# Performance work log

Measured on AMD Instinct MI355X. Metric: run time of the kernel, lower is better.

The kernel has to match this reference:

```python
import jax, jax.numpy as jnp
import numpy as np

N_USER = 150_000
M_ITEM = 30_000
N_NODES = N_USER + M_ITEM
D = 64                      # embedding_dim
N_LAYERS = 3                # gcn_layer_number
E = 600_000                 # user-item interactions (symmetric nnz = 2E)
B = 1024
NUM_RATE, NUM_GENRE, NUM_DIR, NUM_ACT = 6, 25, 2186, 8030
NUM_GENDER, NUM_AGE, NUM_OCC, NUM_ZIP = 2, 7, 21, 3402
H1, H2 = 64, 64             # first/second fc hidden dims
FC1_IN = D * 10


def setup_inputs() -> dict:
    key = jax.random.key(0)
    ks = jax.random.split(key, 24)
    # aux features: 0/1 values are valid indices for every categorical field
    aux_info = jax.random.randint(ks[0], (B, 10246), 0, 2, dtype=jnp.int32)
    user_ids = jax.random.randint(ks[1], (B,), 0, N_USER, dtype=jnp.int32)
    item_ids = jax.random.randint(ks[2], (B,), 0, M_ITEM, dtype=jnp.int32)
    # bipartite graph: random interactions, symmetric normalized adjacency
    u = jax.random.randint(ks[3], (E,), 0, N_USER, dtype=jnp.int32)
    i = jax.random.randint(ks[4], (E,), 0, M_ITEM, dtype=jnp.int32) + N_USER
    graph_row = jnp.concatenate([u, i])
    graph_col = jnpph = jnp.concatenate([i, u]) if False else jnp.concatenate([i, u])
    deg = jax.ops.segment_sum(jnp.ones((2 * E,), jnp.float32), graph_row, num_segments=N_NODES)
    dinv = jnp.where(deg > 0, jax.lax.rsqrt(jnp.maximum(deg, 1.0)), 0.0)
    graph_val = dinv[graph_row] * dinv[graph_col]
    s = 0.1
    nrm = lambda k, shp: (jax.random.normal(k, shp, jnp.float32) * s)
    return {
        "aux_info": aux_info, "user_ids": user_ids, "item_ids": item_ids,
        "graph_row": graph_row, "graph_col": graph_col, "graph_val": graph_val,
        "rate_tab": nrm(ks[5], (NUM_RATE, D)),
        "genre_W": nrm(ks[6], (NUM_GENRE, D)),
        "director_W": nrm(ks[7], (NUM_DIR, D)),
        "actor_W": nrm(ks[8], (NUM_ACT, D)),
        "gender_tab": nrm(ks[9], (NUM_GENDER, D)),
        "age_tab": nrm(ks[10], (NUM_AGE, D)),
        "occ_tab": nrm(ks[11], (NUM_OCC, D)),
        "area_tab": nrm(ks[12], (NUM_ZIP, D)),
        "user_rel": nrm(ks[13], (N_USER, D)),
        "item_rel": nrm(ks[14], (M_ITEM, D)),
        "fc1_W": nrm(ks[15], (FC1_IN, H1)), "fc1_b": jnp.zeros((H1,), jnp.float32),
        "fc2_W": nrm(ks[16], (H1, H2)), "fc2_b": jnp.zeros((H2,), jnp.float32),
        "out_W": nrm(ks[17], (H2, 1)), "out_b": jnp.zeros((1,), jnp.float32),
    }


def _lightgcn(user_rel, item_rel, row, col, val):
    # LightGCN: repeated SpMM D^-1/2 A D^-1/2 @ emb, mean over layer outputs
    emb = jnp.concatenate([user_rel, item_rel], axis=0)      # [N, D]
    acc = emb
    for _ in range(N_LAYERS):
        emb = jax.ops.segment_sum(val[:, None] * emb[col], row, num_segments=N_NODES)
        acc = acc + emb
    light = acc / (N_LAYERS + 1)
    return light[:N_USER], light[N_USER:]


def _multi_hot(idx_int, W):
    x = idx_int.astype(jnp.float32)
    return (x @ W) / jnp.sum(x, axis=1, keepdims=True)


def reference(aux_info, user_ids, item_ids, graph_row, graph_col, graph_val,
              rate_tab, genre_W, director_W, actor_W,
              gender_tab, age_tab, occ_tab, area_tab,
              user_rel, item_rel,
              fc1_W, fc1_b, fc2_W, fc2_b, out_W, out_b):
    rate_idx = aux_info[:, 0]
    genre_idx = aux_info[:, 1:26]
    director_idx = aux_info[:, 26:2212]
    actor_idx = aux_info[:, 2212:10242]
    gender_idx = aux_info[:, 10242]
    age_idx = aux_info[:, 10243]
    occ_idx = aux_info[:, 10244]
    area_idx = aux_info[:, 10245]

    item_emb = jnp.concatenate([
        rate_tab[rate_idx],
        _multi_hot(genre_idx, genre_W),
        _multi_hot(director_idx, director_W),
        _multi_hot(actor_idx, actor_W),
    ], axis=1)                                               # [B, 4D]
    user_emb = jnp.concatenate([
        gender_tab[gender_idx], age_tab[age_idx],
        occ_tab[occ_idx], area_tab[area_idx],
    ], axis=1)                                               # [B, 4D]

    all_users, all_items = _lightgcn(user_rel, item_rel, graph_row, graph_col, graph_val)
    X = jnp.concatenate([item_emb, user_emb,
                         all_users[user_ids], all_items[item_ids]], axis=1)  # [B, 10D]
    X = jax.nn.relu(X @ fc1_W + fc1_b)
    X = jax.nn.relu(X @ fc2_W + fc2_b)
    return X @ out_W + out_b                                 # [B, 1]
```

## Files before the change

### kernel.cpp

```cpp
#include <hip/hip_runtime.h>
#include <hip/hip_bf16.h>
#include <hip/hip_fp16.h>

#define N_USER 150000
#define M_ITEM 30000
#define N_NODES 180000
#define E2 1200000
#define BATCH 1024
#define AUX_W 10246
#define KP_G 32
#define KP_D 2208
#define KP_A 8064
#define NBKT 265
#define WT_BLKS 2576
#define BCNT_BLKS 293
#define MH_BLKS 672
#define CVT_BLKS 5625

typedef __attribute__((ext_vector_type(8))) short short8;
typedef __attribute__((ext_vector_type(8))) unsigned short ushort8_t;
typedef __attribute__((ext_vector_type(4))) float f32x4;

__device__ __forceinline__ int bucket_of(int r) {
    return r < N_USER ? (r >> 10) : 147 + ((r - N_USER) >> 8);
}

__device__ __forceinline__ int detect_f32(const void* probe) {
    float v = __bfloat162float(((const __hip_bfloat16*)probe)[threadIdx.x & 63]);
    unsigned long long m = __ballot(!(fabsf(v) < 1000.0f));
    return __popcll(m) > 8;
}

struct CvtSeg { const void* src; float* dst; int n; int blk0; };
struct CvtBatch { CvtSeg seg[16]; };

__global__ void __launch_bounds__(256) k_prep(CvtBatch cb, int cvtBlks,
                                              const void* Wg, const void* Wd, const void* Wa,
                                              unsigned short* WtG, unsigned short* WtD, unsigned short* WtA,
                                              const int* __restrict__ grow, int* __restrict__ bucket_tot,
                                              int* __restrict__ deg, const void* probe) {
    int blk = blockIdx.x, tid = threadIdx.x;
    if (blk < cvtBlks) {
        int isf32 = detect_f32(probe);
        int si = 0;
        #pragma unroll
        for (int i = 0; i < 16; ++i) if (blk >= cb.seg[i].blk0) si = i;
        const CvtSeg sg = cb.seg[si];
        int i = (blk - sg.blk0) * 256 + tid;
        if (i >= sg.n) return;
        if (isf32) sg.dst[i] = ((const float*)sg.src)[i];
        else       sg.dst[i] = __bfloat162float(((const __hip_bfloat16*)sg.src)[i]);
        return;
    }
    if (blk < cvtBlks + WT_BLKS) {
        int isf32 = detect_f32(probe);
        int t = (blk - cvtBlks) * 256 + tid;
        if (t >= (KP_G + KP_D + KP_A) * 64) return;
        int kp = t >> 6, n = t & 63;
        int k, K; const void* src; unsigned short* dst;
        if (kp < KP_G)              { k = kp;               K = 25;   src = Wg; dst = WtG; }
        else if (kp < KP_G + KP_D)  { k = kp - KP_G;        K = 2186; src = Wd; dst = WtD; }
        else                        { k = kp - KP_G - KP_D; K = 8030; src = Wa; dst = WtA; }
        unsigned short v = 0;
        if (k < K) {
            if (isf32) {
                __hip_bfloat16 h = __float2bfloat16(((const float*)src)[(size_t)k * 64 + n]);
                v = *(unsigned short*)&h;
            } else {
                v = ((const unsigned short*)src)[(size_t)k * 64 + n];
            }
        }
        dst[(((size_t)(k >> 5) * 64 + n) * 4 + ((k >> 3) & 3)) * 8 + (k & 7)] = v;
        return;
    }
    __shared__ int h[NBKT];
    for (int i = tid; i < NBKT; i += 256) h[i] = 0;
    __syncthreads();
    int idx0 = (blk - cvtBlks - WT_BLKS) * 4096;
    #pragma unroll
    for (int k = 0; k < 16; ++k) {
        int i = idx0 + k * 256 + tid;
        if (i < E2) {
            int r = grow[i];
            atomicAdd(&h[bucket_of(r)], 1);
            atomicAdd(&deg[r], 1);
        }
    }
    __syncthreads();
    for (int i = tid; i < NBKT; i += 256) if (h[i]) atomicAdd(&bucket_tot[i], h[i]);
}

__global__ void __launch_bounds__(512) k_bscan(const int* __restrict__ bucket_tot,
                                               int* __restrict__ bucket_base,
                                               int* __restrict__ bucketcur,
                                               const int* __restrict__ deg,
                                               float* __restrict__ dinv, float* __restrict__ dsq,
                                               float* __restrict__ gsc) {
    int tid = threadIdx.x;
    if (blockIdx.x > 0) {
        int r = (blockIdx.x - 1) * 512 + tid;
        float d = (float)deg[r];
        bool nz = d > 0.f;
        dinv[r] = nz ? rsqrtf(d) : 0.f;
        dsq[r]  = nz ? 1.f / d  : 0.f;
        gsc[r]  = nz ? sqrtf(d) : 0.f;
        return;
    }
    __shared__ int s[512];
    s[tid] = (tid < NBKT) ? bucket_tot[tid] : 0;
    __syncthreads();
    for (int off = 1; off < 512; off <<= 1) {
        int v = (tid >= off) ? s[tid - off] : 0;
        __syncthreads();
        s[tid] += v;
        __syncthreads();
    }
    int excl = tid ? s[tid - 1] : 0;
    bucket_base[tid] = excl;
    if (tid < NBKT) bucketcur[tid] = excl;
}

__device__ void mhgemm_body(int blk, const int* __restrict__ aux,
                            const unsigned short* __restrict__ WtG,
                            const unsigned short* __restrict__ WtD,
                            const unsigned short* __restrict__ WtA,
                            float* __restrict__ Xmh, float* __restrict__ cntf) {
    int seg, rb, k0, klen, Kseg, auxoff;
    const unsigned short* Wt;
    if (blk < 16)       { seg = 0; rb = blk;                      k0 = 0;              klen = 25;                  Kseg = 25;   auxoff = 1;    Wt = WtG; }
    else if (blk < 160) { int t = blk - 16;  seg = 1; rb = t & 15; k0 = (t >> 4) * 256; klen = min(256, 2186 - k0); Kseg = 2186; auxoff = 26;   Wt = WtD; }
    else                { int t = blk - 160; seg = 2; rb = t & 15; k0 = (t >> 4) * 256; klen = min(256, 8030 - k0); Kseg = 8030; auxoff = 2212; Wt = WtA; }
    int lane = threadIdx.x & 63, wave = threadIdx.x >> 6;
    int m = lane & 15, quad = lane >> 4;
    int row = rb * 64 + wave * 16 + m;
    const int* arow = aux + (size_t)row * AUX_W + auxoff;

    f32x4 acc0 = {0.f,0.f,0.f,0.f}, acc1 = acc0, acc2 = acc0, acc3 = acc0;
    int isum = 0;
    int nchunk = (klen + 31) >> 5;
    int pa[8], na[8];
    auto lda = [&](int kci, int (&A)[8]) {
        int kb = k0 + kci * 32 + quad * 8;
        if (kb + 8 <= Kseg) {
            #pragma unroll
            for (int j = 0; j < 8; ++j) A[j] = arow[kb + j];
        } else {
            #pragma unroll
            for (int j = 0; j < 8; ++j) A[j] = (kb + j < Kseg) ? arow[kb + j] : 0;
        }
    };
    lda(0, pa);
    for (int kci = 0; kci < nchunk; ++kci) {
        if (kci + 1 < nchunk) lda(kci + 1, na);
        union { unsigned u[4]; short8 s; } af;
        af.u[0] = (unsigned)pa[0] * 16256u + (unsigned)pa[1] * 0x3F800000u;
        af.u[1] = (unsigned)pa[2] * 16256u + (unsigned)pa[3] * 0x3F800000u;
        af.u[2] = (unsigned)pa[4] * 16256u + (unsigned)pa[5] * 0x3F800000u;
        af.u[3] = (unsigned)pa[6] * 16256u + (unsigned)pa[7] * 0x3F800000u;
        isum += pa[0] + pa[1] + pa[2] + pa[3] + pa[4] + pa[5] + pa[6] + pa[7];
        size_t kcg = (size_t)(k0 >> 5) + kci;
        const unsigned short* bp = Wt + ((kcg * 64 + m) * 4 + quad) * 8;
        short8 b0 = *(const short8*)(bp);
        short8 b1 = *(const short8*)(bp + 512);
        short8 b2 = *(const short8*)(bp + 1024);
        short8 b3 = *(const short8*)(bp + 1536);
        acc0 = __builtin_amdgcn_mfma_f32_16x16x32_bf16(af.s, b0, acc0, 0, 0, 0);
        acc1 = __builtin_amdgcn_mfma_f32_16x16x32_bf16(af.s, b1, acc1, 0, 0, 0);
        acc2 = __builtin_amdgcn_mfma_f32_16x16x32_bf16(af.s, b2, acc2, 0, 0, 0);
        acc3 = __builtin_amdgcn_mfma_f32_16x16x32_bf16(af.s, b3, acc3, 0, 0, 0);
        #pragma unroll
        for (int j = 0; j < 8; ++j) pa[j] = na[j];
    }
    float asum = (float)isum;
    asum += __shfl_xor(asum, 16);
    asum += __shfl_xor(asum, 32);
    if (quad == 0) atomicAdd(&cntf[seg * BATCH + row], asum);
    float* xbase = Xmh + ((size_t)seg * BATCH + rb * 64 + wave * 16 + quad * 4) * 64;
    #pragma unroll
    for (int reg = 0; reg < 4; ++reg) {
        float* xr = xbase + (size_t)reg * 64;
        atomicAdd(&xr[ 0 + m], acc0[reg]);
        atomicAdd(&xr[16 + m], acc1[reg]);
        atomicAdd(&xr[32 + m], acc2[reg]);
        atomicAdd(&xr[48 + m], acc3[reg]);
    }
}

__global__ void __launch_bounds__(256) k_p1(const int* __restrict__ grow, const int* __restrict__ gcol,
                                            int* __restrict__ bucketcur, int2* __restrict__ binned,
                                            const int* __restrict__ aux,
                                            const unsigned short* __restrict__ WtG,
                                            const unsigned short* __restrict__ WtD,
                                            const unsigned short* __restrict__ WtA,
                                            float* __restrict__ Xmh, float* __restrict__ cntf,
                                            const void* rawU, const void* rawI,
                                            const float* __restrict__ dinv,
                                            __half* __restrict__ emb) {
    int blk = blockIdx.x;
    if (blk < MH_BLKS) {
        mhgemm_body(blk, aux, WtG, WtD, WtA, Xmh, cntf);
        return;
    }
    if (blk < MH_BLKS + BCNT_BLKS) {
        __shared__ int h1[NBKT], base1[NBKT];
        int tid = threadIdx.x;
        for (int i = tid; i < NBKT; i += 256) h1[i] = 0;
        __syncthreads();
        int idx0 = (blk - MH_BLKS) * 4096;
        int r[16], c[16];
        #pragma unroll
        for (int k = 0; k < 16; ++k) {
            int i = idx0 + k * 256 + tid;
            if (i < E2) {
                r[k] = grow[i]; c[k] = gcol[i];
                atomicAdd(&h1[bucket_of(r[k])], 1);
            } else r[k] = -1;
        }
        __syncthreads();
        for (int i = tid; i < NBKT; i += 256) {
            base1[i] = h1[i] ? atomicAdd(&bucketcur[i], h1[i]) : 0;
            h1[i] = 0;
        }
        __syncthreads();
        #pragma unroll
        for (int k = 0; k < 16; ++k) {
            if (r[k] >= 0) {
                int b = bucket_of(r[k]);
                int p = base1[b] + atomicAdd(&h1[b], 1);
                binned[p] = make_int2(r[k], c[k]);
            }
        }
        return;
    }
    int isf32 = detect_f32(rawU);
    int q = (blk - MH_BLKS - BCNT_BLKS) * 256 + threadIdx.x;
    if (q >= N_NODES * 8) return;
    int r = q >> 3;
    const void* src; size_t qq;
    if (r < N_USER) { src = rawU; qq = (size_t)q; }
    else            { src = rawI; qq = (size_t)q - (size_t)N_USER * 8; }
    float d = dinv[r];
    float f[8];
    if (isf32) {
        float4 a = ((const float4*)src)[qq * 2], b = ((const float4*)src)[qq * 2 + 1];
        f[0]=a.x; f[1]=a.y; f[2]=a.z; f[3]=a.w; f[4]=b.x; f[5]=b.y; f[6]=b.z; f[7]=b.w;
    } else {
        ushort8_t u = ((const ushort8_t*)src)[qq];
        #pragma unroll
        for (int i = 0; i < 8; ++i) {
            unsigned short us = u[i];
            f[i] = __bfloat162float(*(__hip_bfloat16*)&us);
        }
    }
    ushort8_t o;
    #pragma unroll
    for (int i = 0; i < 8; ++i) {
        __half h = __float2half(f[i] * d);
        o[i] = *(unsigned short*)&h;
    }
    ((ushort8_t*)emb)[(size_t)q] = o;
}

__global__ void __launch_bounds__(256) k_p2(const int2* __restrict__ binned, const int* __restrict__ bb,
                                            int* __restrict__ cols, int2* __restrict__ moffs) {
    __shared__ int h[1024];
    __shared__ int ws2[256];
    int b = blockIdx.x, tid = threadIdx.x;
    int r0, r1;
    if (b < 147) { r0 = b << 10; r1 = min((b + 1) << 10, N_USER); }
    else         { r0 = N_USER + ((b - 147) << 8); r1 = min(N_USER + ((b - 146) << 8), N_NODES); }
    int s0 = bb[b], e0 = bb[b + 1];
    for (int i = tid; i < 1024; i += 256) h[i] = 0;
    __syncthreads();
    for (int j = s0 + tid; j < e0; j += 256) atomicAdd(&h[binned[j].x - r0], 1);
    __syncthreads();
    int t0 = tid * 4;
    int a0 = h[t0], a1 = h[t0 + 1], a2 = h[t0 + 2], a3 = h[t0 + 3];
    ws2[tid] = a0 + a1 + a2 + a3;
    __syncthreads();
    for (int off = 1; off < 256; off <<= 1) {
        int v = (tid >= off) ? ws2[tid - off] : 0;
        __syncthreads();
        ws2[tid] += v;
        __syncthreads();
    }
    int excl = tid ? ws2[tid - 1] : 0;
    int ex[4] = { excl, excl + a0, excl + a0 + a1, excl + a0 + a1 + a2 };
    int ac[4] = { a0, a1, a2, a3 };
    #pragma unroll
    for (int i = 0; i < 4; ++i) {
        int row = r0 + t0 + i;
        if (row < r1) moffs[row] = make_int2(s0 + ex[i], s0 + ex[i] + ac[i]);
        h[t0 + i] = ex[i];
    }
    __syncthreads();
    for (int j = s0 + tid; j < e0; j += 256) {
        int2 e = binned[j];
        int p = s0 + atomicAdd(&h[e.x - r0], 1);
        cols[p] = e.y << 7;
    }
}

__global__ void __launch_bounds__(256, 8) k_spmv(const __half* __restrict__ src, __half* __restrict__ dst,
                                                 const int2* __restrict__ moffs_in, const int* __restrict__ cols,
                                                 const float* __restrict__ dsq,
                                                 int spmvN, float* __restrict__ tacc,
                                                 const int* __restrict__ uids, const int* __restrict__ iids,
                                                 const float* __restrict__ gsc,
                                                 const void* rawU, const void* rawI,
                                                 int2* __restrict__ moffs2, int xmode) {
    int tid = threadIdx.x, lane = tid & 63;
    int blk = blockIdx.x;
    if (blk >= spmvN) {
        if (xmode == 1) {
            int t = (blk - spmvN) * 4 + (tid >> 6);
            int r = (t < BATCH) ? uids[t] : (N_USER + iids[t - BATCH]);
            tacc[(size_t)t * 64 + lane] += __half2float(src[(size_t)r * 64 + lane]) * gsc[r];
            return;
        }
        if (blk < spmvN + 512) {
            int t = (blk - spmvN) * 4 + (tid >> 6);
            int r = (t < BATCH) ? uids[t] : (N_USER + iids[t - BATCH]);
            int2 se = moffs_in[r];
            if (lane == 0) moffs2[r] = se;
            for (int j = se.x + lane; j < se.y; j += 64) {
                int c = (unsigned)cols[j] >> 7;
                moffs2[c] = moffs_in[c];
            }
            return;
        }
        {
            int isf32 = detect_f32(rawU);
            int t = (blk - spmvN - 512) * 4 + (tid >> 6);
            const void* s; size_t ri;
            if (t < BATCH) { s = rawU; ri = (size_t)uids[t]; }
            else           { s = rawI; ri = (size_t)iids[t - BATCH]; }
            float v;
            if (isf32) v = ((const float*)s)[ri * 64 + lane];
            else       v = __bfloat162float(((const __hip_bfloat16*)s)[ri * 64 + lane]);
            tacc[(size_t)t * 64 + lane] = v;
            return;
        }
    }
    int wid8 = blk * 4 + (tid >> 6);
    int g = lane >> 3, l8 = lane & 7;
    int r = wid8 * 8 + g;
    int2 se = moffs_in[r];
    int s = se.x, e = se.y;
    const char* sb = (const char*)src + (l8 << 4);
    float2 a0 = {0.f,0.f}, a1 = a0, a2 = a0, a3 = a0;
    int j0 = s;
    for (; j0 + 4 <= e; j0 += 4) {
        int c[4];
        #pragma unroll
        for (int u = 0; u < 4; ++u) c[u] = cols[j0 + u];
        float4 rv[4];
        #pragma unroll
        for (int u = 0; u < 4; ++u) rv[u] = *(const float4*)(sb + (size_t)(unsigned)c[u]);
        #pragma unroll
        for (int u = 0; u < 4; ++u) {
            const __half2* h = (const __half2*)&rv[u];
            float2 f0 = __half22float2(h[0]), f1 = __half22float2(h[1]);
            float2 f2 = __half22float2(h[2]), f3 = __half22float2(h[3]);
            a0.x += f0.x; a0.y += f0.y; a1.x += f1.x; a1.y += f1.y;
            a2.x += f2.x; a2.y += f2.y; a3.x += f3.x; a3.y += f3.y;
        }
    }
    if (j0 < e) {
        int c[4]; float w[4];
        #pragma unroll
        for (int u = 0; u < 4; ++u) {
            int j = j0 + u;
            c[u] = cols[min(j, e - 1)];
            w[u] = (j < e) ? 1.f : 0.f;
        }
        float4 rv[4];
        #pragma unroll
        for (int u = 0; u < 4; ++u) rv[u] = *(const float4*)(sb + (size_t)(unsigned)c[u]);
        #pragma unroll
        for (int u = 0; u < 4; ++u) {
            const __half2* h = (const __half2*)&rv[u];
            float2 f0 = __half22float2(h[0]), f1 = __half22float2(h[1]);
            float2 f2 = __half22float2(h[2]), f3 = __half22float2(h[3]);
            a0.x = fmaf(w[u], f0.x, a0.x); a0.y = fmaf(w[u], f0.y, a0.y);
            a1.x = fmaf(w[u], f1.x, a1.x); a1.y = fmaf(w[u], f1.y, a1.y);
            a2.x = fmaf(w[u], f2.x, a2.x); a2.y = fmaf(w[u], f2.y, a2.y);
            a3.x = fmaf(w[u], f3.x, a3.x); a3.y = fmaf(w[u], f3.y, a3.y);
        }
    }
    if (e > s) {
        float d = dsq[r];
        float4 ov;
        __half2* op = (__half2*)&ov;
        op[0] = __floats2half2_rn(a0.x * d, a0.y * d);
        op[1] = __floats2half2_rn(a1.x * d, a1.y * d);
        op[2] = __floats2half2_rn(a2.x * d, a2.y * d);
        op[3] = __floats2half2_rn(a3.x * d, a3.y * d);
        *(float4*)((char*)dst + ((size_t)r << 7) + (l8 << 4)) = ov;
    }
}

__global__ void __launch_bounds__(256) k_spmv3(const __half* __restrict__ src, float* __restrict__ tacc,
                                               const int2* __restrict__ moffs, const int* __restrict__ cols,
                                               const float* __restrict__ dinv, const float* __restrict__ gsc,
                                               const int* __restrict__ uids, const int* __restrict__ iids) {
    int tid = threadIdx.x, lane = tid & 63;
    int t = blockIdx.x * 4 + (tid >> 6);
    if (t >= 2048) return;
    int r = (t < BATCH) ? uids[t] : (N_USER + iids[t - BATCH]);
    int2 se = moffs[r];
    int s = se.x, e = se.y;
    int p = lane & 31, ep = lane >> 5;
    const char* sb = (const char*)src + (p << 2);
    float ax = 0.f, ay = 0.f;
    int j0 = s;
    for (; j0 + 16 <= e; j0 += 16) {
        int c[8];
        #pragma unroll
        for (int u = 0; u < 8; ++u) c[u] = cols[j0 + 2 * u + ep];
        float2 v[8];
        #pragma unroll
        for (int u = 0; u < 8; ++u) v[u] = __half22float2(*(const __half2*)(sb + (size_t)(unsigned)c[u]));
        #pragma unroll
        for (int u = 0; u < 8; ++u) { ax += v[u].x; ay += v[u].y; }
    }
    if (j0 + 8 <= e) {
        int c[4];
        #pragma unroll
        for (int u = 0; u < 4; ++u) c[u] = cols[j0 + 2 * u + ep];
        float2 v[4];
        #pragma unroll
        for (int u = 0; u < 4; ++u) v[u] = __half22float2(*(const __half2*)(sb + (size_t)(unsigned)c[u]));
        #pragma unroll
        for (int u = 0; u < 4; ++u) { ax += v[u].x; ay += v[u].y; }
        j0 += 8;
    }
    if (j0 + 4 <= e) {
        int c0 = cols[j0 + ep], c1 = cols[j0 + 2 + ep];
        float2 v0 = __half22float2(*(const __half2*)(sb + (size_t)(unsigned)c0));
        float2 v1 = __half22float2(*(const __half2*)(sb + (size_t)(unsigned)c1));
        ax += v0.x + v1.x; ay += v0.y + v1.y;
        j0 += 4;
    }
    if (j0 < e) {
        int j1 = j0 + ep, j2 = j0 + 2 + ep;
        int c0 = cols[min(j1, e - 1)], c1 = cols[min(j2, e - 1)];
        float w0 = (j1 < e) ? 1.f : 0.f, w1 = (j2 < e) ? 1.f : 0.f;
        float2 v0 = __half22float2(*(const __half2*)(sb + (size_t)(unsigned)c0));
        float2 v1 = __half22float2(*(const __half2*)(sb + (size_t)(unsigned)c1));
        ax = fmaf(w0, v0.x, ax); ay = fmaf(w0, v0.y, ay);
        ax = fmaf(w1, v1.x, ax); ay = fmaf(w1, v1.y, ay);
    }
    ax += __shfl_xor(ax, 32);
    ay += __shfl_xor(ay, 32);
    if (ep == 0) {
        float2 self = __half22float2(*(const __half2*)((const char*)src + ((size_t)r << 7) + (p << 2)));
        float di = dinv[r], g = gsc[r];
        float* tp = tacc + (size_t)t * 64 + (p << 1);
        tp[0] += di * ax + g * self.x;
        tp[1] += di * ay + g * self.y;
    }
}

__global__ void __launch_bounds__(256) k_mlp(const int* __restrict__ aux,
                                             const float* __restrict__ ratef, const float* __restrict__ genderf,
                                             const float* __restrict__ agef, const float* __restrict__ occf,
                                             const float* __restrict__ areaf, const float* __restrict__ tacc,
                                             const float* __restrict__ Xmh, const float* __restrict__ cntf,
                                             const float* __restrict__ W1, const float* __restrict__ b1,
                                             const float* __restrict__ W2, const float* __restrict__ b2,
                                             const float* __restrict__ Wo, const float* __restrict__ bo,
                                             void* __restrict__ out, const void* probe) {
    __shared__ float sx[4][640];
    __shared__ float sh[4][64];
    int isf32 = detect_f32(probe);
    int lane = threadIdx.x & 63, w = threadIdx.x >> 6;
    int b = blockIdx.x * 4 + w;
    const int* arow = aux + (size_t)b * AUX_W;
    float* xr = sx[w];
    xr[0   + lane] = ratef[arow[0] * 64 + lane];
    xr[64  + lane] = Xmh[((size_t)0 * BATCH + b) * 64 + lane] / cntf[0 * BATCH + b];
    xr[128 + lane] = Xmh[((size_t)1 * BATCH + b) * 64 + lane] / cntf[1 * BATCH + b];
    xr[192 + lane] = Xmh[((size_t)2 * BATCH + b) * 64 + lane] / cntf[2 * BATCH + b];
    xr[256 + lane] = genderf[arow[10242] * 64 + lane];
    xr[320 + lane] = agef[arow[10243] * 64 + lane];
    xr[384 + lane] = occf[arow[10244] * 64 + lane];
    xr[448 + lane] = areaf[arow[10245] * 64 + lane];
    xr[512 + lane] = tacc[(size_t)b * 64 + lane] * 0.25f;
    xr[576 + lane] = tacc[(size_t)(BATCH + b) * 64 + lane] * 0.25f;
    float acc = b1[lane];
    #pragma unroll 8
    for (int k = 0; k < 640; ++k) acc += xr[k] * W1[(size_t)k * 64 + lane];
    float h1 = fmaxf(acc, 0.f);
    sh[w][lane] = h1;
    float acc2 = b2[lane];
    #pragma unroll 8
    for (int j = 0; j < 64; ++j) acc2 += sh[w][j] * W2[(size_t)j * 64 + lane];
    float h2 = fmaxf(acc2, 0.f);
    float p = h2 * Wo[lane];
    #pragma unroll
    for (int off = 32; off; off >>= 1) p += __shfl_down(p, off);
    if (lane == 0) {
        float r = p + bo[0];
        if (isf32) ((float*)out)[b] = r;
        else       ((__hip_bfloat16*)out)[b] = __float2bfloat16(r);
    }
}

extern "C" void kernel_launch(void* const* d_in, const int* in_sizes, int n_in,
                              void* d_out, int out_size, void* d_ws, size_t ws_size,
                              hipStream_t stream) {
    const int* aux  = (const int*)d_in[0];
    const int* uids = (const int*)d_in[1];
    const int* iids = (const int*)d_in[2];
    const int* grow = (const int*)d_in[3];
    const int* gcol = (const int*)d_in[4];

    char* p = (char*)d_ws;
    auto alloc = [&](size_t bytes) -> char* {
        char* r = p;
        p += (bytes + 255) / 256 * 256;
        return r;
    };
    int*   bucket_tot  = (int*)alloc(512 * 4);
    float* Xmh         = (float*)alloc((size_t)3 * BATCH * 64 * 4);
    float* cntf        = (float*)alloc((size_t)3 * BATCH * 4);
    int2*  moffs2      = (int2*)alloc((size_t)180224 * 8);
    int*   deg         = (int*)alloc((size_t)180224 * 4);
    char*  zero_end    = p;
    int*   bucket_base = (int*)alloc(512 * 4);
    int*   bucketcur   = (int*)alloc(512 * 4);
    int2*  moffs       = (int2*)alloc((size_t)180224 * 8);
    float* dinv        = (float*)alloc((size_t)180224 * 4);
    float* dsq         = (float*)alloc((size_t)180224 * 4);
    float* gsc         = (float*)alloc((size_t)180224 * 4);
    int2*  binned      = (int2*)alloc((size_t)E2 * 8);
    int*   cols        = (int*)alloc((size_t)E2 * 4);
    __half* embA       = (__half*)alloc((size_t)N_NODES * 64 * 2);
    __half* embB       = (__half*)alloc((size_t)N_NODES * 64 * 2);
    float* tacc        = (float*)alloc((size_t)2048 * 64 * 4);
    unsigned short* WtG = (unsigned short*)alloc((size_t)KP_G * 64 * 2);
    unsigned short* WtD = (unsigned short*)alloc((size_t)KP_D * 64 * 2);
    unsigned short* WtA = (unsigned short*)alloc((size_t)KP_A * 64 * 2);
    float* ratef   = (float*)alloc(384 * 4);
    float* genderf = (float*)alloc(128 * 4);
    float* agef    = (float*)alloc(448 * 4);
    float* occf    = (float*)alloc(1344 * 4);
    float* areaf   = (float*)alloc((size_t)217728 * 4);
    float* fc1W    = (float*)alloc((size_t)40960 * 4);
    float* fc1b    = (float*)alloc(64 * 4);
    float* fc2W    = (float*)alloc(4096 * 4);
    float* fc2b    = (float*)alloc(64 * 4);
    float* outW    = (float*)alloc(64 * 4);
    float* outb    = (float*)alloc(4);

    const void* probe = d_in[14];

    hipMemsetAsync(bucket_tot, 0, (size_t)(zero_end - (char*)bucket_tot), stream);

    CvtBatch cb;
    int blk = 0, si = 0;
    auto addseg = [&](const void* s, float* d, int n) {
        cb.seg[si].src = s; cb.seg[si].dst = d; cb.seg[si].n = n; cb.seg[si].blk0 = blk;
        blk += (n + 255) / 256; ++si;
    };
    addseg(d_in[6],  ratef,   384);
    addseg(d_in[10], genderf, 128);
    addseg(d_in[11], agef,    448);
    addseg(d_in[12], occf,    1344);
    addseg(d_in[13], areaf,   217728);
    addseg(d_in[16], fc1W,   40960);
    addseg(d_in[17], fc1b,   64);
    addseg(d_in[18], fc2W,   4096);
    addseg(d_in[19], fc2b,   64);
    addseg(d_in[20], outW,   64);
    addseg(d_in[21], outb,   1);
    for (int i = si; i < 16; ++i) { cb.seg[i].src = nullptr; cb.seg[i].dst = nullptr; cb.seg[i].n = 0; cb.seg[i].blk0 = 0x7fffffff; }
    const int cvtBlks = blk;
    hipLaunchKernelGGL(k_prep, dim3(cvtBlks + WT_BLKS + BCNT_BLKS), dim3(256), 0, stream,
                       cb, cvtBlks, d_in[7], d_in[8], d_in[9], WtG, WtD, WtA, grow, bucket_tot, deg, probe);

    hipLaunchKernelGGL(k_bscan, dim3(353), dim3(512), 0, stream,
                       bucket_tot, bucket_base, bucketcur, deg, dinv, dsq, gsc);

    hipLaunchKernelGGL(k_p1, dim3(MH_BLKS + BCNT_BLKS + CVT_BLKS), dim3(256), 0, stream,
                       grow, gcol, bucketcur, binned, aux, WtG, WtD, WtA, Xmh, cntf,
                       d_in[14], d_in[15], dinv, embA);

    hipLaunchKernelGGL(k_p2, dim3(NBKT), dim3(256), 0, stream, binned, bucket_base, cols, moffs);

    const int spmvN = N_NODES / 32;
    hipLaunchKernelGGL(k_spmv, dim3(spmvN + 1024), dim3(256), 0, stream,
                       embA, embB, moffs, cols, dsq, spmvN, tacc, uids, iids, gsc,
                       d_in[14], d_in[15], moffs2, 0);
    hipLaunchKernelGGL(k_spmv, dim3(spmvN + 512), dim3(256), 0, stream,
                       embB, embA, moffs2, cols, dsq, spmvN, tacc, uids, iids, gsc,
                       d_in[14], d_in[15], moffs2, 1);
    hipLaunchKernelGGL(k_spmv3, dim3(2048 / 4), dim3(256), 0, stream,
                       embA, tacc, moffs, cols, dinv, gsc, uids, iids);

    hipLaunchKernelGGL(k_mlp, dim3(BATCH / 4), dim3(256), 0, stream,
                       aux, ratef, genderf, agef, occf, areaf, tacc, Xmh, cntf,
                       fc1W, fc1b, fc2W, fc2b, outW, outb, d_out, probe);
}
```

Measured before the change: 327.2 us.

## Derive node degrees from CSR build instead of global atomics

Drops the per-edge global atomicAdd on the degree array in the prep kernel and instead computes dinv, dsq and gsc inside the bucket-local CSR build kernel, where per-row counts are already known. The bucket-count blocks move to the front of the prep grid, the scan kernel shrinks to one block, and the embedding conversion is split out of k_p1 into its own kernel launched after k_p2. This removes 1.2M contended global atomics and a degree pass, at the cost of one extra kernel launch and serializing the embedding conversion behind the CSR build.

Result: faster. 290.4 us (-11.2%).

```diff
diff --git a/kernel.cpp b/kernel.cpp
--- a/kernel.cpp
+++ b/kernel.cpp
@@ -38,23 +38,38 @@
                                               const void* Wg, const void* Wd, const void* Wa,
                                               unsigned short* WtG, unsigned short* WtD, unsigned short* WtA,
                                               const int* __restrict__ grow, int* __restrict__ bucket_tot,
-                                              int* __restrict__ deg, const void* probe) {
+                                              const void* probe) {
     int blk = blockIdx.x, tid = threadIdx.x;
-    if (blk < cvtBlks) {
+    if (blk < BCNT_BLKS) {
+        __shared__ int h[NBKT];
+        for (int i = tid; i < NBKT; i += 256) h[i] = 0;
+        __syncthreads();
+        int idx0 = blk * 4096;
+        #pragma unroll
+        for (int k = 0; k < 16; ++k) {
+            int i = idx0 + k * 256 + tid;
+            if (i < E2) atomicAdd(&h[bucket_of(grow[i])], 1);
+        }
+        __syncthreads();
+        for (int i = tid; i < NBKT; i += 256) if (h[i]) atomicAdd(&bucket_tot[i], h[i]);
+        return;
+    }
+    if (blk < BCNT_BLKS + cvtBlks) {
         int isf32 = detect_f32(probe);
+        int cblk = blk - BCNT_BLKS;
         int si = 0;
         #pragma unroll
-        for (int i = 0; i < 16; ++i) if (blk >= cb.seg[i].blk0) si = i;
+        for (int i = 0; i < 16; ++i) if (cblk >= cb.seg[i].blk0) si = i;
         const CvtSeg sg = cb.seg[si];
-        int i = (blk - sg.blk0) * 256 + tid;
+        int i = (cblk - sg.blk0) * 256 + tid;
         if (i >= sg.n) return;
         if (isf32) sg.dst[i] = ((const float*)sg.src)[i];
         else       sg.dst[i] = __bfloat162float(((const __hip_bfloat16*)sg.src)[i]);
         return;
     }
-    if (blk < cvtBlks + WT_BLKS) {
+    {
         int isf32 = detect_f32(probe);
-        int t = (blk - cvtBlks) * 256 + tid;
+        int t = (blk - BCNT_BLKS - cvtBlks) * 256 + tid;
         if (t >= (KP_G + KP_D + KP_A) * 64) return;
         int kp = t >> 6, n = t & 63;
         int k, K; const void* src; unsigned short* dst;
@@ -71,42 +86,14 @@
             }
         }
         dst[(((size_t)(k >> 5) * 64 + n) * 4 + ((k >> 3) & 3)) * 8 + (k & 7)] = v;
-        return;
-    }
-    __shared__ int h[NBKT];
-    for (int i = tid; i < NBKT; i += 256) h[i] = 0;
-    __syncthreads();
-    int idx0 = (blk - cvtBlks - WT_BLKS) * 4096;
-    #pragma unroll
-    for (int k = 0; k < 16; ++k) {
-        int i = idx0 + k * 256 + tid;
-        if (i < E2) {
-            int r = grow[i];
-            atomicAdd(&h[bucket_of(r)], 1);
-            atomicAdd(&deg[r], 1);
-        }
-    }
-    __syncthreads();
-    for (int i = tid; i < NBKT; i += 256) if (h[i]) atomicAdd(&bucket_tot[i], h[i]);
+    }
 }
 
 __global__ void __launch_bounds__(512) k_bscan(const int* __restrict__ bucket_tot,
                                                int* __restrict__ bucket_base,
-                                               int* __restrict__ bucketcur,
-                                               const int* __restrict__ deg,
-                                               float* __restrict__ dinv, float* __restrict__ dsq,
-                                               float* __restrict__ gsc) {
+                                               int* __restrict__ bucketcur) {
+    __shared__ int s[512];
     int tid = threadIdx.x;
-    if (blockIdx.x > 0) {
-        int r = (blockIdx.x - 1) * 512 + tid;
-        float d = (float)deg[r];
-        bool nz = d > 0.f;
-        dinv[r] = nz ? rsqrtf(d) : 0.f;
-        dsq[r]  = nz ? 1.f / d  : 0.f;
-        gsc[r]  = nz ? sqrtf(d) : 0.f;
-        return;
-    }
-    __shared__ int s[512];
     s[tid] = (tid < NBKT) ? bucket_tot[tid] : 0;
     __syncthreads();
     for (int off = 1; off < 512; off <<= 1) {
@@ -192,48 +179,96 @@
                                             const unsigned short* __restrict__ WtG,
                                             const unsigned short* __restrict__ WtD,
                                             const unsigned short* __restrict__ WtA,
-                                            float* __restrict__ Xmh, float* __restrict__ cntf,
-                                            const void* rawU, const void* rawI,
-                                            const float* __restrict__ dinv,
-                                            __half* __restrict__ emb) {
+                                            float* __restrict__ Xmh, float* __restrict__ cntf) {
     int blk = blockIdx.x;
     if (blk < MH_BLKS) {
         mhgemm_body(blk, aux, WtG, WtD, WtA, Xmh, cntf);
         return;
     }
-    if (blk < MH_BLKS + BCNT_BLKS) {
-        __shared__ int h1[NBKT], base1[NBKT];
-        int tid = threadIdx.x;
-        for (int i = tid; i < NBKT; i += 256) h1[i] = 0;
+    __shared__ int h1[NBKT], base1[NBKT];
+    int tid = threadIdx.x;
+    for (int i = tid; i < NBKT; i += 256) h1[i] = 0;
+    __syncthreads();
+    int idx0 = (blk - MH_BLKS) * 4096;
+    int r[16], c[16];
+    #pragma unroll
+    for (int k = 0; k < 16; ++k) {
+        int i = idx0 + k * 256 + tid;
+        if (i < E2) {
+            r[k] = grow[i]; c[k] = gcol[i];
+            atomicAdd(&h1[bucket_of(r[k])], 1);
+        } else r[k] = -1;
+    }
+    __syncthreads();
+    for (int i = tid; i < NBKT; i += 256) {
+        base1[i] = h1[i] ? atomicAdd(&bucketcur[i], h1[i]) : 0;
+        h1[i] = 0;
+    }
+    __syncthreads();
+    #pragma unroll
+    for (int k = 0; k < 16; ++k) {
+        if (r[k] >= 0) {
+            int b = bucket_of(r[k]);
+            int p = base1[b] + atomicAdd(&h1[b], 1);
+            binned[p] = make_int2(r[k], c[k]);
+        }
+    }
+}
+
+__global__ void __launch_bounds__(256) k_p2(const int2* __restrict__ binned, const int* __restrict__ bb,
+                                            int* __restrict__ cols, int2* __restrict__ moffs,
+                                            float* __restrict__ dinv, float* __restrict__ dsq,
+                                            float* __restrict__ gsc) {
+    __shared__ int h[1024];
+    __shared__ int ws2[256];
+    int b = blockIdx.x, tid = threadIdx.x;
+    int r0, r1;
+    if (b < 147) { r0 = b << 10; r1 = min((b + 1) << 10, N_USER); }
+    else         { r0 = N_USER + ((b - 147) << 8); r1 = min(N_USER + ((b - 146) << 8), N_NODES); }
+    int s0 = bb[b], e0 = bb[b + 1];
+    for (int i = tid; i < 1024; i += 256) h[i] = 0;
+    __syncthreads();
+    for (int j = s0 + tid; j < e0; j += 256) atomicAdd(&h[binned[j].x - r0], 1);
+    __syncthreads();
+    int t0 = tid * 4;
+    int a0 = h[t0], a1 = h[t0 + 1], a2 = h[t0 + 2], a3 = h[t0 + 3];
+    ws2[tid] = a0 + a1 + a2 + a3;
+    __syncthreads();
+    for (int off = 1; off < 256; off <<= 1) {
+        int v = (tid >= off) ? ws2[tid - off] : 0;
         __syncthreads();
-        int idx0 = (blk - MH_BLKS) * 4096;
-        int r[16], c[16];
-        #pragma unroll
-        for (int k = 0; k < 16; ++k) {
-            int i = idx0 + k * 256 + tid;
-            if (i < E2) {
-                r[k] = grow[i]; c[k] = gcol[i];
-                atomicAdd(&h1[bucket_of(r[k])], 1);
-            } else r[k] = -1;
-        }
+        ws2[tid] += v;
         __syncthreads();
-        for (int i = tid; i < NBKT; i += 256) {
-            base1[i] = h1[i] ? atomicAdd(&bucketcur[i], h1[i]) : 0;
-            h1[i] = 0;
-        }
-        __syncthreads();
-        #pragma unroll
-        for (int k = 0; k < 16; ++k) {
-            if (r[k] >= 0) {
-                int b = bucket_of(r[k]);
-                int p = base1[b] + atomicAdd(&h1[b], 1);
-                binned[p] = make_int2(r[k], c[k]);
-            }
-        }
-        return;
-    }
+    }
+    int excl = tid ? ws2[tid - 1] : 0;
+    int ex[4] = { excl, excl + a0, excl + a0 + a1, excl + a0 + a1 + a2 };
+    int ac[4] = { a0, a1, a2, a3 };
+    #pragma unroll
+    for (int i = 0; i < 4; ++i) {
+        int row = r0 + t0 + i;
+        if (row < r1) {
+            moffs[row] = make_int2(s0 + ex[i], s0 + ex[i] + ac[i]);
+            float deg = (float)ac[i];
+            bool nz = deg > 0.f;
+            dinv[row] = nz ? rsqrtf(deg) : 0.f;
+            dsq[row]  = nz ? 1.f / deg  : 0.f;
+            gsc[row]  = nz ? sqrtf(deg) : 0.f;
+        }
+        h[t0 + i] = ex[i];
+    }
+    __syncthreads();
+    for (int j = s0 + tid; j < e0; j += 256) {
+        int2 e = binned[j];
+        int p = s0 + atomicAdd(&h[e.x - r0], 1);
+        cols[p] = e.y << 7;
+    }
+}
+
+__global__ void __launch_bounds__(256) k_cvt(const void* rawU, const void* rawI,
+                                             const float* __restrict__ dinv,
+                                             __half* __restrict__ emb) {
     int isf32 = detect_f32(rawU);
-    int q = (blk - MH_BLKS - BCNT_BLKS) * 256 + threadIdx.x;
+    int q = blockIdx.x * 256 + threadIdx.x;
     if (q >= N_NODES * 8) return;
     int r = q >> 3;
     const void* src; size_t qq;
@@ -259,46 +294,6 @@
         o[i] = *(unsigned short*)&h;
     }
     ((ushort8_t*)emb)[(size_t)q] = o;
-}
-
-__global__ void __launch_bounds__(256) k_p2(const int2* __restrict__ binned, const int* __restrict__ bb,
-                                            int* __restrict__ cols, int2* __restrict__ moffs) {
-    __shared__ int h[1024];
-    __shared__ int ws2[256];
-    int b = blockIdx.x, tid = threadIdx.x;
-    int r0, r1;
-    if (b < 147) { r0 = b << 10; r1 = min((b + 1) << 10, N_USER); }
-    else         { r0 = N_USER + ((b - 147) << 8); r1 = min(N_USER + ((b - 146) << 8), N_NODES); }
-    int s0 = bb[b], e0 = bb[b + 1];
-    for (int i = tid; i < 1024; i += 256) h[i] = 0;
-    __syncthreads();
-    for (int j = s0 + tid; j < e0; j += 256) atomicAdd(&h[binned[j].x - r0], 1);
-    __syncthreads();
-    int t0 = tid * 4;
-    int a0 = h[t0], a1 = h[t0 + 1], a2 = h[t0 + 2], a3 = h[t0 + 3];
-    ws2[tid] = a0 + a1 + a2 + a3;
-    __syncthreads();
-    for (int off = 1; off < 256; off <<= 1) {
-        int v = (tid >= off) ? ws2[tid - off] : 0;
-        __syncthreads();
-        ws2[tid] += v;
-        __syncthreads();
-    }
-    int excl = tid ? ws2[tid - 1] : 0;
-    int ex[4] = { excl, excl + a0, excl + a0 + a1, excl + a0 + a1 + a2 };
-    int ac[4] = { a0, a1, a2, a3 };
-    #pragma unroll
-    for (int i = 0; i < 4; ++i) {
-        int row = r0 + t0 + i;
-        if (row < r1) moffs[row] = make_int2(s0 + ex[i], s0 + ex[i] + ac[i]);
-        h[t0 + i] = ex[i];
-    }
-    __syncthreads();
-    for (int j = s0 + tid; j < e0; j += 256) {
-        int2 e = binned[j];
-        int p = s0 + atomicAdd(&h[e.x - r0], 1);
-        cols[p] = e.y << 7;
-    }
 }
 
 __global__ void __launch_bounds__(256, 8) k_spmv(const __half* __restrict__ src, __half* __restrict__ dst,
@@ -526,7 +521,6 @@
     float* Xmh         = (float*)alloc((size_t)3 * BATCH * 64 * 4);
     float* cntf        = (float*)alloc((size_t)3 * BATCH * 4);
     int2*  moffs2      = (int2*)alloc((size_t)180224 * 8);
-    int*   deg         = (int*)alloc((size_t)180224 * 4);
     char*  zero_end    = p;
     int*   bucket_base = (int*)alloc(512 * 4);
     int*   bucketcur   = (int*)alloc(512 * 4);
@@ -577,17 +571,16 @@
     addseg(d_in[21], outb,   1);
     for (int i = si; i < 16; ++i) { cb.seg[i].src = nullptr; cb.seg[i].dst = nullptr; cb.seg[i].n = 0; cb.seg[i].blk0 = 0x7fffffff; }
     const int cvtBlks = blk;
-    hipLaunchKernelGGL(k_prep, dim3(cvtBlks + WT_BLKS + BCNT_BLKS), dim3(256), 0, stream,
-                       cb, cvtBlks, d_in[7], d_in[8], d_in[9], WtG, WtD, WtA, grow, bucket_tot, deg, probe);
-
-    hipLaunchKernelGGL(k_bscan, dim3(353), dim3(512), 0, stream,
-                       bucket_tot, bucket_base, bucketcur, deg, dinv, dsq, gsc);
-
-    hipLaunchKernelGGL(k_p1, dim3(MH_BLKS + BCNT_BLKS + CVT_BLKS), dim3(256), 0, stream,
-                       grow, gcol, bucketcur, binned, aux, WtG, WtD, WtA, Xmh, cntf,
+    hipLaunchKernelGGL(k_prep, dim3(BCNT_BLKS + cvtBlks + WT_BLKS), dim3(256), 0, stream,
+                       cb, cvtBlks, d_in[7], d_in[8], d_in[9], WtG, WtD, WtA, grow, bucket_tot, probe);
+
+    hipLaunchKernelGGL(k_bscan, dim3(1), dim3(512), 0, stream, bucket_tot, bucket_base, bucketcur);
+    hipLaunchKernelGGL(k_p1, dim3(MH_BLKS + BCNT_BLKS), dim3(256), 0, stream,
+                       grow, gcol, bucketcur, binned, aux, WtG, WtD, WtA, Xmh, cntf);
+    hipLaunchKernelGGL(k_p2, dim3(NBKT), dim3(256), 0, stream, binned, bucket_base, cols, moffs, dinv, dsq, gsc);
+
+    hipLaunchKernelGGL(k_cvt, dim3(CVT_BLKS), dim3(256), 0, stream,
                        d_in[14], d_in[15], dinv, embA);
-
-    hipLaunchKernelGGL(k_p2, dim3(NBKT), dim3(256), 0, stream, binned, bucket_base, cols, moffs);
 
     const int spmvN = N_NODES / 32;
     hipLaunchKernelGGL(k_spmv, dim3(spmvN + 1024), dim3(256), 0, stream,
```
